# Optimization experiments

Hardware: AMD Instinct MI355X
Metric: run time of the kernel (lower is better)

## Reference

```python
import jax, jax.numpy as jnp
import numpy as np

N_NODES = 10000
N_EDGES = 16384
D = 128            # node_in_dim == out_dim == edge_attr_dim == hidden_dim


def setup_inputs() -> dict:
    key = jax.random.key(0)
    ks = jax.random.split(key, 9)
    s = 1.0 / np.sqrt(D)
    x = jax.random.normal(ks[0], (N_NODES, D), dtype=jnp.float32)
    edge_index = jax.random.randint(ks[1], (2, N_EDGES), 0, N_NODES, dtype=jnp.int64)
    edge_attr = jax.random.normal(ks[2], (N_EDGES, D), dtype=jnp.float32)
    # edge_net: MLP 128 -> 128 (ReLU) -> 128*128
    w1 = jax.random.normal(ks[3], (D, D), dtype=jnp.float32) * s
    b1 = jnp.zeros((D,), dtype=jnp.float32)
    w2 = jax.random.normal(ks[4], (D, D * D), dtype=jnp.float32) * s
    b2 = jnp.zeros((D * D,), dtype=jnp.float32)
    # NNConv root weight and bias
    root = jax.random.normal(ks[5], (D, D), dtype=jnp.float32) * s
    bias = jnp.zeros((D,), dtype=jnp.float32)
    return {"x": x, "edge_index": edge_index, "edge_attr": edge_attr,
            "w1": w1, "b1": b1, "w2": w2, "b2": b2, "root": root, "bias": bias}


def reference(x, edge_index, edge_attr, w1, b1, w2, b2, root, bias):
    src, dst = edge_index[0], edge_index[1]
    # edge_net -> per-edge weight matrices [E, D, D]
    h = jax.nn.relu(edge_attr @ w1 + b1)
    w_edge = (h @ w2 + b2).reshape(-1, D, D)
    # gather source features, per-edge matvec: [E, D]
    x_j = x[src]
    msg = jnp.einsum('ei,eio->eo', x_j, w_edge)
    # scatter-mean into destination nodes
    seg_sum = jax.ops.segment_sum(msg, dst, num_segments=N_NODES)
    cnt = jax.ops.segment_sum(jnp.ones((msg.shape[0],), msg.dtype), dst,
                              num_segments=N_NODES)
    aggr = seg_sum / jnp.maximum(cnt, 1.0)[:, None]
    # NNConv root transform + bias
    conv_out = aggr + x @ root + bias
    # residual + exact GELU (torch nn.GELU default)
    return x + jax.nn.gelu(conv_out, approximate=False)
```

## Files before the change

kernel.cpp:

```cpp
#include <hip/hip_runtime.h>
#include <math.h>

#define D 128
#define NNODES 10000
#define NEDGES 16384
#define PADR 136
#define MAXDEG 16

typedef short short8 __attribute__((ext_vector_type(8)));
typedef float floatx4 __attribute__((ext_vector_type(4)));

__device__ __forceinline__ float bf2f(unsigned short u) {
  union { unsigned u; float f; } v; v.u = ((unsigned)u) << 16; return v.f;
}
__device__ __forceinline__ unsigned short f2bf(float f) {
  union { float f; unsigned u; } v; v.f = f;
  return (unsigned short)((v.u + 0x7FFFu + ((v.u >> 16) & 1u)) >> 16);
}
__device__ __forceinline__ float bflo(unsigned u) {
  union { unsigned u; float f; } v; v.u = u << 16; return v.f;
}
__device__ __forceinline__ float bfhi(unsigned u) {
  union { unsigned u; float f; } v; v.u = u & 0xFFFF0000u; return v.f;
}
__device__ __forceinline__ short8 pack8(float4 a, float4 b) {
  short8 r;
  r[0] = (short)f2bf(a.x); r[1] = (short)f2bf(a.y);
  r[2] = (short)f2bf(a.z); r[3] = (short)f2bf(a.w);
  r[4] = (short)f2bf(b.x); r[5] = (short)f2bf(b.y);
  r[6] = (short)f2bf(b.z); r[7] = (short)f2bf(b.w);
  return r;
}

__global__ __launch_bounds__(256) void k2_prep(
    const float* __restrict__ w2, const float* __restrict__ b2,
    const float* __restrict__ w1, const float* __restrict__ root,
    unsigned short* __restrict__ w2t, unsigned short* __restrict__ w1t,
    unsigned short* __restrict__ rootT) {
  __shared__ float L[32][129];
  const int t = threadIdx.x;
  const int bid = blockIdx.x;
  const float* __restrict__ src;
  unsigned short* dst;
  int o0;
  if (bid < 516) {
    const int k = bid >> 2;
    o0 = (bid & 3) * 32;
    src = (k < D) ? (w2 + (long)k * (D * D)) : b2;
    dst = w2t + (long)k * (D * PADR);
  } else if (bid < 520) {
    o0 = (bid - 516) * 32; src = w1; dst = w1t;
  } else {
    o0 = (bid - 520) * 32; src = root; dst = rootT;
  }
#pragma unroll
  for (int r = 0; r < 16; ++r) {
    int idx = r * 256 + t;
    int i = idx >> 5, oc = idx & 31;
    L[oc][i] = src[i * D + o0 + oc];
  }
  __syncthreads();
#pragma unroll
  for (int r = 0; r < 8; ++r) {
    int p = r * 256 + t;
    int oc = p >> 6, i2 = (p & 63) * 2;
    unsigned v = (unsigned)f2bf(L[oc][i2]) | ((unsigned)f2bf(L[oc][i2 + 1]) << 16);
    *(unsigned*)(dst + ((o0 + oc) * PADR + i2)) = v;
  }
}

__global__ __launch_bounds__(256) void k1_edge(
    const float* __restrict__ x, const int* __restrict__ eidx,
    const float* __restrict__ ea, const unsigned short* __restrict__ w1t,
    const float* __restrict__ b1, unsigned short* __restrict__ hT,
    unsigned short* __restrict__ xjb, int* __restrict__ cnt,
    int* __restrict__ elist) {
  const int t = threadIdx.x;
  const int e0 = blockIdx.x * 64;
  if (t < 64) {
    const int e = e0 + t;
    const int d = eidx[NEDGES + e];
    const int pos = atomicAdd(&cnt[d], 1);
    if (pos < MAXDEG) elist[d * MAXDEG + pos] = e;
  }
#pragma unroll 4
  for (int r = 0; r < 16; ++r) {
    int idx = r * 256 + t, e = idx >> 6, i2 = (idx & 63) * 2;
    const int s = eidx[e0 + e];
    const float2 v = *(const float2*)(x + (long)s * D + i2);
    unsigned p = (unsigned)f2bf(v.x) | ((unsigned)f2bf(v.y) << 16);
    *(unsigned*)(xjb + ((e0 + e) * PADR + i2)) = p;
  }
  const int lane = t & 63, w = t >> 6, lo = lane & 15, hi = lane >> 4;
  short8 af[4];
#pragma unroll
  for (int ks = 0; ks < 4; ++ks) {
    const float* p0 = ea + (long)(e0 + w * 16 + lo) * D + ks * 32 + hi * 8;
    af[ks] = pack8(*(const float4*)p0, *(const float4*)(p0 + 4));
  }
  floatx4 acc[8];
#pragma unroll
  for (int nt = 0; nt < 8; ++nt) acc[nt] = (floatx4){0.f, 0.f, 0.f, 0.f};
#pragma unroll
  for (int ks = 0; ks < 4; ++ks) {
    const int ib = ks * 32 + hi * 8;
#pragma unroll
    for (int nt = 0; nt < 8; ++nt) {
      const short8 bf_ = *(const short8*)&w1t[(nt * 16 + lo) * PADR + ib];
      acc[nt] = __builtin_amdgcn_mfma_f32_16x16x32_bf16(af[ks], bf_, acc[nt], 0, 0, 0);
    }
  }
#pragma unroll
  for (int nt = 0; nt < 8; ++nt) {
    const int ko = nt * 16 + lo;
    const float b1v = b1[ko];
    float v0 = fmaxf(acc[nt][0] + b1v, 0.f);
    float v1 = fmaxf(acc[nt][1] + b1v, 0.f);
    float v2 = fmaxf(acc[nt][2] + b1v, 0.f);
    float v3 = fmaxf(acc[nt][3] + b1v, 0.f);
    uint2 pk;
    pk.x = (unsigned)f2bf(v0) | ((unsigned)f2bf(v1) << 16);
    pk.y = (unsigned)f2bf(v2) | ((unsigned)f2bf(v3) << 16);
    *(uint2*)(hT + (ko * NEDGES + e0 + w * 16 + hi * 4)) = pk;
  }
  if (t < 64) hT[128 * NEDGES + e0 + t] = 0x3F80;
}

__global__ __launch_bounds__(256, 3) void k3_msg(
    const unsigned short* __restrict__ w2t,
    const unsigned short* __restrict__ xjb,
    const unsigned short* __restrict__ hT,
    unsigned short* __restrict__ msgout) {
  __shared__ float hLT[65 * 128];
  const int t = threadIdx.x;
  const int b = blockIdx.x;
  const int kh = b & 1;
  const int oq = (b >> 1) & 3;
  const int eg = b >> 3;
  const int e0 = eg * 128;
  const int o0 = oq * 32;
  const int kbase = kh * 64;
  const int kcnt = kh ? 65 : 64;
  const int lane = t & 63, wv = t >> 6;
  const int lo = lane & 15, hi = lane >> 4;
  const int we = (wv >> 1) * 64;
  const int wo = (wv & 1) * 16;

  for (int idx = t; idx < kcnt * 64; idx += 256) {
    const int kk = idx >> 6, e2 = (idx & 63) * 2;
    const unsigned u = *(const unsigned*)&hT[(long)(kbase + kk) * NEDGES + e0 + e2];
    const int ebase = kk * 128;
#pragma unroll
    for (int q = 0; q < 2; ++q) {
      const int e = e2 + q;
      hLT[ebase + ((e >> 6) << 6) + ((e & 15) << 2) + ((e >> 4) & 3)] =
          q ? bfhi(u) : bflo(u);
    }
  }

  short8 xf[4][4];
#pragma unroll
  for (int ne = 0; ne < 4; ++ne)
#pragma unroll
    for (int ks = 0; ks < 4; ++ks)
      xf[ne][ks] = *(const short8*)&xjb[(long)(e0 + we + ne * 16 + lo) * PADR + ks * 32 + hi * 8];
  __syncthreads();

  const long kstride = (long)D * PADR;
  const unsigned short* ap = w2t + (long)kbase * kstride + (long)(o0 + wo + lo) * PADR + hi * 8;
  const float* hp = hLT + we + lo * 4;
  short8 a0[4], a1[4];
#pragma unroll
  for (int ks = 0; ks < 4; ++ks) a0[ks] = *(const short8*)(ap + ks * 32);
#pragma unroll
  for (int ks = 0; ks < 4; ++ks) a1[ks] = *(const short8*)(ap + kstride + ks * 32);
  floatx4 msg[4];
#pragma unroll
  for (int ne = 0; ne < 4; ++ne) msg[ne] = (floatx4){0.f, 0.f, 0.f, 0.f};

  auto body = [&](short8* fr, int k) {
    const floatx4 h4 = *(const floatx4*)(hp + k * 128);
    floatx4 P[4];
#pragma unroll
    for (int ne = 0; ne < 4; ++ne) P[ne] = (floatx4){0.f, 0.f, 0.f, 0.f};
#pragma unroll
    for (int ks = 0; ks < 4; ++ks)
#pragma unroll
      for (int ne = 0; ne < 4; ++ne)
        P[ne] = __builtin_amdgcn_mfma_f32_16x16x32_bf16(fr[ks], xf[ne][ks], P[ne], 0, 0, 0);
#pragma unroll
    for (int ne = 0; ne < 4; ++ne)
#pragma unroll
      for (int r = 0; r < 4; ++r) msg[ne][r] += h4[ne] * P[ne][r];
  };

  const int kpairs = kcnt >> 1;
  for (int j = 0; j < kpairs; ++j) {
    const int k = j * 2;
    body(a0, k);
    {
      const int kp = (k + 2 < kcnt) ? k + 2 : 0;
#pragma unroll
      for (int ks = 0; ks < 4; ++ks)
        a0[ks] = *(const short8*)(ap + (long)kp * kstride + ks * 32);
    }
    body(a1, k + 1);
    {
      const int kp = (k + 3 < kcnt) ? k + 3 : 0;
#pragma unroll
      for (int ks = 0; ks < 4; ++ks)
        a1[ks] = *(const short8*)(ap + (long)kp * kstride + ks * 32);
    }
  }
  if (kcnt & 1) body(a0, kcnt - 1);

#pragma unroll
  for (int ne = 0; ne < 4; ++ne) {
    const long e = e0 + we + ne * 16 + lo;
    uint2 pk;
    pk.x = (unsigned)f2bf(msg[ne][0]) | ((unsigned)f2bf(msg[ne][1]) << 16);
    pk.y = (unsigned)f2bf(msg[ne][2]) | ((unsigned)f2bf(msg[ne][3]) << 16);
    *(uint2*)(msgout + ((long)kh * NEDGES + e) * D + o0 + wo + hi * 4) = pk;
  }
}

__global__ __launch_bounds__(256) void k4_out(
    const float* __restrict__ x, const unsigned short* __restrict__ rootT,
    const float* __restrict__ bias, const unsigned short* __restrict__ msg,
    const int* __restrict__ cnt, const int* __restrict__ elist,
    float* __restrict__ out) {
  __shared__ float segL[64 * 132];
  const int t = threadIdx.x;
  const int n0 = blockIdx.x * 64;
  {
    const int ln = t >> 2;
    const int n = n0 + ln;
    const int oq = (t & 3) * 32;
    float a[32];
#pragma unroll
    for (int i = 0; i < 32; ++i) a[i] = 0.f;
    if (n < NNODES) {
      const int deg = min(cnt[n], MAXDEG);
      for (int j = 0; j < deg; ++j) {
        const int e = elist[n * MAXDEG + j];
        const unsigned short* r0 = msg + (long)e * D + oq;
        const unsigned short* r1 = r0 + (long)NEDGES * D;
#pragma unroll
        for (int q = 0; q < 4; ++q) {
          const uint4 u0 = *(const uint4*)(r0 + q * 8);
          const uint4 u1 = *(const uint4*)(r1 + q * 8);
          a[q * 8 + 0] += bflo(u0.x) + bflo(u1.x);
          a[q * 8 + 1] += bfhi(u0.x) + bfhi(u1.x);
          a[q * 8 + 2] += bflo(u0.y) + bflo(u1.y);
          a[q * 8 + 3] += bfhi(u0.y) + bfhi(u1.y);
          a[q * 8 + 4] += bflo(u0.z) + bflo(u1.z);
          a[q * 8 + 5] += bfhi(u0.z) + bfhi(u1.z);
          a[q * 8 + 6] += bflo(u0.w) + bflo(u1.w);
          a[q * 8 + 7] += bfhi(u0.w) + bfhi(u1.w);
        }
      }
    }
#pragma unroll
    for (int q = 0; q < 8; ++q)
      *(float4*)&segL[ln * 132 + oq + q * 4] =
          (float4){a[q * 4], a[q * 4 + 1], a[q * 4 + 2], a[q * 4 + 3]};
  }
  __syncthreads();
  const int lane = t & 63, w = t >> 6, lo = lane & 15, hi = lane >> 4;
  const int nrow = n0 + w * 16 + lo;
  short8 af[4];
#pragma unroll
  for (int ks = 0; ks < 4; ++ks) {
    if (nrow < NNODES) {
      const float* p0 = x + (long)nrow * D + ks * 32 + hi * 8;
      af[ks] = pack8(*(const float4*)p0, *(const float4*)(p0 + 4));
    } else {
      af[ks] = (short8){0, 0, 0, 0, 0, 0, 0, 0};
    }
  }
  floatx4 acc[8];
#pragma unroll
  for (int nt = 0; nt < 8; ++nt) acc[nt] = (floatx4){0.f, 0.f, 0.f, 0.f};
#pragma unroll
  for (int ks = 0; ks < 4; ++ks) {
    const int ib = ks * 32 + hi * 8;
#pragma unroll
    for (int nt = 0; nt < 8; ++nt) {
      const short8 bf_ = *(const short8*)&rootT[(nt * 16 + lo) * PADR + ib];
      acc[nt] = __builtin_amdgcn_mfma_f32_16x16x32_bf16(af[ks], bf_, acc[nt], 0, 0, 0);
    }
  }
  float dinv[4];
#pragma unroll
  for (int r = 0; r < 4; ++r) {
    const int n = n0 + w * 16 + hi * 4 + r;
    dinv[r] = (n < NNODES) ? 1.0f / fmaxf((float)cnt[n], 1.0f) : 0.f;
  }
#pragma unroll
  for (int nt = 0; nt < 8; ++nt) {
    const int co = nt * 16 + lo;
    const float bv = bias[co];
#pragma unroll
    for (int r = 0; r < 4; ++r) {
      const int n = n0 + w * 16 + hi * 4 + r;
      if (n < NNODES) {
        const float aggr = segL[(w * 16 + hi * 4 + r) * 132 + co] * dinv[r];
        const float v = acc[nt][r] + aggr + bv;
        const float ge = 0.5f * v * (1.0f + erff(v * 0.70710678f));
        out[(long)n * D + co] = x[(long)n * D + co] + ge;
      }
    }
  }
}

extern "C" void kernel_launch(void* const* d_in, const int* in_sizes, int n_in,
                              void* d_out, int out_size, void* d_ws, size_t ws_size,
                              hipStream_t stream) {
  (void)in_sizes; (void)n_in; (void)out_size; (void)ws_size;
  const float* x    = (const float*)d_in[0];
  const int*   eidx = (const int*)d_in[1];
  const float* ea   = (const float*)d_in[2];
  const float* w1   = (const float*)d_in[3];
  const float* b1   = (const float*)d_in[4];
  const float* w2   = (const float*)d_in[5];
  const float* b2   = (const float*)d_in[6];
  const float* root = (const float*)d_in[7];
  const float* bias = (const float*)d_in[8];
  float* out = (float*)d_out;
  char* ws = (char*)d_ws;
  unsigned short* hT    = (unsigned short*)(ws + 0);
  unsigned short* xjb   = (unsigned short*)(ws + 4227072);
  unsigned short* w2t   = (unsigned short*)(ws + 8683520);
  unsigned short* msg   = (unsigned short*)(ws + 13174784);
  int*            cnt   = (int*)(ws + 21563392);
  int*            elist = (int*)(ws + 21603392);
  unsigned short* w1t   = (unsigned short*)(ws + 22243392);
  unsigned short* rootT = (unsigned short*)(ws + 22278208);
  hipMemsetAsync(cnt, 0, 40000, stream);
  hipLaunchKernelGGL(k2_prep, dim3(524), dim3(256), 0, stream,
                     w2, b2, w1, root, w2t, w1t, rootT);
  hipLaunchKernelGGL(k1_edge, dim3(NEDGES / 64), dim3(256), 0, stream,
                     x, eidx, ea, w1t, b1, hT, xjb, cnt, elist);
  hipLaunchKernelGGL(k3_msg, dim3(1024), dim3(256), 0, stream,
                     w2t, xjb, hT, msg);
  hipLaunchKernelGGL(k4_out, dim3((NNODES + 63) / 64), dim3(256), 0, stream,
                     x, rootT, bias, msg, cnt, elist, out);
}
```

Before: 185.5 us.

## Split k3 over input halves instead of hidden halves, widen k4 grid by output quarters

The message kernel now splits work across blocks by input-dimension half, not hidden-unit half. Each block runs all 129 hidden units with half the K-depth MFMAs. The hidden activations are stored in LDS as bf16 rather than fp32 to fit, and occupancy rises to 4 blocks per SM, with s_setprio set around the MFMA burst. The output kernel is split into four output-column quarters per 64-node tile, giving four times as many blocks with fewer registers each. The cost is that the x rows, root weights and edge lists are read redundantly by each quarter.

```diff
diff --git a/kernel.cpp b/kernel.cpp
--- a/kernel.cpp
+++ b/kernel.cpp
@@ -9,6 +9,7 @@
 
 typedef short short8 __attribute__((ext_vector_type(8)));
 typedef float floatx4 __attribute__((ext_vector_type(4)));
+typedef unsigned short ushortx4 __attribute__((ext_vector_type(4)));
 
 __device__ __forceinline__ float bf2f(unsigned short u) {
   union { unsigned u; float f; } v; v.u = ((unsigned)u) << 16; return v.f;
@@ -126,93 +127,93 @@
   if (t < 64) hT[128 * NEDGES + e0 + t] = 0x3F80;
 }
 
-__global__ __launch_bounds__(256, 3) void k3_msg(
+__global__ __launch_bounds__(256, 4) void k3_msg(
     const unsigned short* __restrict__ w2t,
     const unsigned short* __restrict__ xjb,
     const unsigned short* __restrict__ hT,
     unsigned short* __restrict__ msgout) {
-  __shared__ float hLT[65 * 128];
+  __shared__ unsigned short hLT[129 * 128];
   const int t = threadIdx.x;
   const int b = blockIdx.x;
-  const int kh = b & 1;
+  const int ih = b & 1;
   const int oq = (b >> 1) & 3;
   const int eg = b >> 3;
   const int e0 = eg * 128;
   const int o0 = oq * 32;
-  const int kbase = kh * 64;
-  const int kcnt = kh ? 65 : 64;
   const int lane = t & 63, wv = t >> 6;
   const int lo = lane & 15, hi = lane >> 4;
   const int we = (wv >> 1) * 64;
   const int wo = (wv & 1) * 16;
 
-  for (int idx = t; idx < kcnt * 64; idx += 256) {
+  for (int idx = t; idx < 129 * 64; idx += 256) {
     const int kk = idx >> 6, e2 = (idx & 63) * 2;
-    const unsigned u = *(const unsigned*)&hT[(long)(kbase + kk) * NEDGES + e0 + e2];
-    const int ebase = kk * 128;
-#pragma unroll
-    for (int q = 0; q < 2; ++q) {
-      const int e = e2 + q;
-      hLT[ebase + ((e >> 6) << 6) + ((e & 15) << 2) + ((e >> 4) & 3)] =
-          q ? bfhi(u) : bflo(u);
-    }
-  }
-
-  short8 xf[4][4];
+    const unsigned u = *(const unsigned*)&hT[(long)kk * NEDGES + e0 + e2];
+    const int kb = kk * 128 + ((e2 >> 6) << 6);
+    hLT[kb + ((e2 & 15) << 2) + ((e2 >> 4) & 3)] = (unsigned short)(u & 0xFFFFu);
+    const int e3 = e2 + 1;
+    hLT[kb + ((e3 & 15) << 2) + ((e3 >> 4) & 3)] = (unsigned short)(u >> 16);
+  }
+
+  short8 xf[4][2];
 #pragma unroll
   for (int ne = 0; ne < 4; ++ne)
 #pragma unroll
-    for (int ks = 0; ks < 4; ++ks)
-      xf[ne][ks] = *(const short8*)&xjb[(long)(e0 + we + ne * 16 + lo) * PADR + ks * 32 + hi * 8];
+    for (int ks = 0; ks < 2; ++ks)
+      xf[ne][ks] = *(const short8*)&xjb[(long)(e0 + we + ne * 16 + lo) * PADR +
+                                        ih * 64 + ks * 32 + hi * 8];
   __syncthreads();
 
   const long kstride = (long)D * PADR;
-  const unsigned short* ap = w2t + (long)kbase * kstride + (long)(o0 + wo + lo) * PADR + hi * 8;
-  const float* hp = hLT + we + lo * 4;
-  short8 a0[4], a1[4];
-#pragma unroll
-  for (int ks = 0; ks < 4; ++ks) a0[ks] = *(const short8*)(ap + ks * 32);
-#pragma unroll
-  for (int ks = 0; ks < 4; ++ks) a1[ks] = *(const short8*)(ap + kstride + ks * 32);
+  const unsigned short* ap = w2t + (long)(o0 + wo + lo) * PADR + ih * 64 + hi * 8;
+  const unsigned short* hp = hLT + we + lo * 4;
+  short8 a0[2], a1[2];
+#pragma unroll
+  for (int ks = 0; ks < 2; ++ks) a0[ks] = *(const short8*)(ap + ks * 32);
+#pragma unroll
+  for (int ks = 0; ks < 2; ++ks) a1[ks] = *(const short8*)(ap + kstride + ks * 32);
   floatx4 msg[4];
 #pragma unroll
   for (int ne = 0; ne < 4; ++ne) msg[ne] = (floatx4){0.f, 0.f, 0.f, 0.f};
 
   auto body = [&](short8* fr, int k) {
-    const floatx4 h4 = *(const floatx4*)(hp + k * 128);
+    const ushortx4 hu = *(const ushortx4*)(hp + k * 128);
     floatx4 P[4];
 #pragma unroll
     for (int ne = 0; ne < 4; ++ne) P[ne] = (floatx4){0.f, 0.f, 0.f, 0.f};
-#pragma unroll
-    for (int ks = 0; ks < 4; ++ks)
+    __builtin_amdgcn_s_setprio(1);
+#pragma unroll
+    for (int ks = 0; ks < 2; ++ks)
 #pragma unroll
       for (int ne = 0; ne < 4; ++ne)
         P[ne] = __builtin_amdgcn_mfma_f32_16x16x32_bf16(fr[ks], xf[ne][ks], P[ne], 0, 0, 0);
+    __builtin_amdgcn_s_setprio(0);
+    float hv[4];
+#pragma unroll
+    for (int ne = 0; ne < 4; ++ne) hv[ne] = bf2f(hu[ne]);
 #pragma unroll
     for (int ne = 0; ne < 4; ++ne)
 #pragma unroll
-      for (int r = 0; r < 4; ++r) msg[ne][r] += h4[ne] * P[ne][r];
+      for (int r = 0; r < 4; ++r) msg[ne][r] += hv[ne] * P[ne][r];
   };
 
-  const int kpairs = kcnt >> 1;
-  for (int j = 0; j < kpairs; ++j) {
+  for (int j = 0; j < 64; ++j) {
     const int k = j * 2;
     body(a0, k);
     {
-      const int kp = (k + 2 < kcnt) ? k + 2 : 0;
-#pragma unroll
-      for (int ks = 0; ks < 4; ++ks)
+      const int kp = k + 2;
+#pragma unroll
+      for (int ks = 0; ks < 2; ++ks)
         a0[ks] = *(const short8*)(ap + (long)kp * kstride + ks * 32);
     }
     body(a1, k + 1);
     {
-      const int kp = (k + 3 < kcnt) ? k + 3 : 0;
-#pragma unroll
-      for (int ks = 0; ks < 4; ++ks)
+      const int kp = (k + 3 < 129) ? k + 3 : 0;
+#pragma unroll
+      for (int ks = 0; ks < 2; ++ks)
         a1[ks] = *(const short8*)(ap + (long)kp * kstride + ks * 32);
     }
   }
-  if (kcnt & 1) body(a0, kcnt - 1);
+  body(a0, 128);
 
 #pragma unroll
   for (int ne = 0; ne < 4; ++ne) {
@@ -220,7 +221,7 @@
     uint2 pk;
     pk.x = (unsigned)f2bf(msg[ne][0]) | ((unsigned)f2bf(msg[ne][1]) << 16);
     pk.y = (unsigned)f2bf(msg[ne][2]) | ((unsigned)f2bf(msg[ne][3]) << 16);
-    *(uint2*)(msgout + ((long)kh * NEDGES + e) * D + o0 + wo + hi * 4) = pk;
+    *(uint2*)(msgout + ((long)ih * NEDGES + e) * D + o0 + wo + hi * 4) = pk;
   }
 }
 
@@ -229,41 +230,38 @@
     const float* __restrict__ bias, const unsigned short* __restrict__ msg,
     const int* __restrict__ cnt, const int* __restrict__ elist,
     float* __restrict__ out) {
-  __shared__ float segL[64 * 132];
+  __shared__ float segL[64 * 36];
   const int t = threadIdx.x;
-  const int n0 = blockIdx.x * 64;
+  const int bid = blockIdx.x;
+  const int n0 = (bid >> 2) * 64;
+  const int oq = (bid & 3) * 32;
   {
     const int ln = t >> 2;
     const int n = n0 + ln;
-    const int oq = (t & 3) * 32;
-    float a[32];
-#pragma unroll
-    for (int i = 0; i < 32; ++i) a[i] = 0.f;
+    const int os = (t & 3) * 8;
+    float a[8];
+#pragma unroll
+    for (int i = 0; i < 8; ++i) a[i] = 0.f;
     if (n < NNODES) {
       const int deg = min(cnt[n], MAXDEG);
       for (int j = 0; j < deg; ++j) {
         const int e = elist[n * MAXDEG + j];
-        const unsigned short* r0 = msg + (long)e * D + oq;
+        const unsigned short* r0 = msg + (long)e * D + oq + os;
         const unsigned short* r1 = r0 + (long)NEDGES * D;
-#pragma unroll
-        for (int q = 0; q < 4; ++q) {
-          const uint4 u0 = *(const uint4*)(r0 + q * 8);
-          const uint4 u1 = *(const uint4*)(r1 + q * 8);
-          a[q * 8 + 0] += bflo(u0.x) + bflo(u1.x);
-          a[q * 8 + 1] += bfhi(u0.x) + bfhi(u1.x);
-          a[q * 8 + 2] += bflo(u0.y) + bflo(u1.y);
-          a[q * 8 + 3] += bfhi(u0.y) + bfhi(u1.y);
-          a[q * 8 + 4] += bflo(u0.z) + bflo(u1.z);
-          a[q * 8 + 5] += bfhi(u0.z) + bfhi(u1.z);
-          a[q * 8 + 6] += bflo(u0.w) + bflo(u1.w);
-          a[q * 8 + 7] += bfhi(u0.w) + bfhi(u1.w);
-        }
+        const uint4 u0 = *(const uint4*)r0;
+        const uint4 u1 = *(const uint4*)r1;
+        a[0] += bflo(u0.x) + bflo(u1.x);
+        a[1] += bfhi(u0.x) + bfhi(u1.x);
+        a[2] += bflo(u0.y) + bflo(u1.y);
+        a[3] += bfhi(u0.y) + bfhi(u1.y);
+        a[4] += bflo(u0.z) + bflo(u1.z);
+        a[5] += bfhi(u0.z) + bfhi(u1.z);
+        a[6] += bflo(u0.w) + bflo(u1.w);
+        a[7] += bfhi(u0.w) + bfhi(u1.w);
       }
     }
-#pragma unroll
-    for (int q = 0; q < 8; ++q)
-      *(float4*)&segL[ln * 132 + oq + q * 4] =
-          (float4){a[q * 4], a[q * 4 + 1], a[q * 4 + 2], a[q * 4 + 3]};
+    *(float4*)&segL[ln * 36 + os] = (float4){a[0], a[1], a[2], a[3]};
+    *(float4*)&segL[ln * 36 + os + 4] = (float4){a[4], a[5], a[6], a[7]};
   }
   __syncthreads();
   const int lane = t & 63, w = t >> 6, lo = lane & 15, hi = lane >> 4;
@@ -278,15 +276,15 @@
       af[ks] = (short8){0, 0, 0, 0, 0, 0, 0, 0};
     }
   }
-  floatx4 acc[8];
-#pragma unroll
-  for (int nt = 0; nt < 8; ++nt) acc[nt] = (floatx4){0.f, 0.f, 0.f, 0.f};
+  floatx4 acc[2];
+#pragma unroll
+  for (int nt = 0; nt < 2; ++nt) acc[nt] = (floatx4){0.f, 0.f, 0.f, 0.f};
 #pragma unroll
   for (int ks = 0; ks < 4; ++ks) {
     const int ib = ks * 32 + hi * 8;
 #pragma unroll
-    for (int nt = 0; nt < 8; ++nt) {
-      const short8 bf_ = *(const short8*)&rootT[(nt * 16 + lo) * PADR + ib];
+    for (int nt = 0; nt < 2; ++nt) {
+      const short8 bf_ = *(const short8*)&rootT[(oq + nt * 16 + lo) * PADR + ib];
       acc[nt] = __builtin_amdgcn_mfma_f32_16x16x32_bf16(af[ks], bf_, acc[nt], 0, 0, 0);
     }
   }
@@ -297,14 +295,15 @@
     dinv[r] = (n < NNODES) ? 1.0f / fmaxf((float)cnt[n], 1.0f) : 0.f;
   }
 #pragma unroll
-  for (int nt = 0; nt < 8; ++nt) {
-    const int co = nt * 16 + lo;
+  for (int nt = 0; nt < 2; ++nt) {
+    const int col = nt * 16 + lo;
+    const int co = oq + col;
     const float bv = bias[co];
 #pragma unroll
     for (int r = 0; r < 4; ++r) {
       const int n = n0 + w * 16 + hi * 4 + r;
       if (n < NNODES) {
-        const float aggr = segL[(w * 16 + hi * 4 + r) * 132 + co] * dinv[r];
+        const float aggr = segL[(w * 16 + hi * 4 + r) * 36 + col] * dinv[r];
         const float v = acc[nt][r] + aggr + bv;
         const float ge = 0.5f * v * (1.0f + erff(v * 0.70710678f));
         out[(long)n * D + co] = x[(long)n * D + co] + ge;
@@ -343,6 +342,6 @@
                      x, eidx, ea, w1t, b1, hT, xjb, cnt, elist);
   hipLaunchKernelGGL(k3_msg, dim3(1024), dim3(256), 0, stream,
                      w2t, xjb, hT, msg);
-  hipLaunchKernelGGL(k4_out, dim3((NNODES + 63) / 64), dim3(256), 0, stream,
+  hipLaunchKernelGGL(k4_out, dim3(628), dim3(256), 0, stream,
                      x, rootT, bias, msg, cnt, elist, out);
 }
```

New measurement: 194.2 us. 1.05x slower.

## Scatter messages with float atomics in msg kernel instead of edge-list gather

Applied to the files above, without the earlier changes.

The message kernel now atomically adds each per-edge message into a float aggregation buffer indexed by destination node. This removes the bf16 message buffer, the per-node edge lists and the gather loop in the output kernel. The hidden-activation tile in shared memory is stored as bf16 instead of fp32, and the memset is folded into the prep kernel, which also zeroes the aggregation buffer. In exchange it issues many global float atomics (two k-halves and repeated destinations contend), the summation order is no longer deterministic, and the old cap of 16 edges per node no longer applies.

```diff
diff --git a/kernel.cpp b/kernel.cpp
--- a/kernel.cpp
+++ b/kernel.cpp
@@ -5,10 +5,10 @@
 #define NNODES 10000
 #define NEDGES 16384
 #define PADR 136
-#define MAXDEG 16
 
 typedef short short8 __attribute__((ext_vector_type(8)));
 typedef float floatx4 __attribute__((ext_vector_type(4)));
+typedef unsigned short ushortx4 __attribute__((ext_vector_type(4)));
 
 __device__ __forceinline__ float bf2f(unsigned short u) {
   union { unsigned u; float f; } v; v.u = ((unsigned)u) << 16; return v.f;
@@ -36,10 +36,18 @@
     const float* __restrict__ w2, const float* __restrict__ b2,
     const float* __restrict__ w1, const float* __restrict__ root,
     unsigned short* __restrict__ w2t, unsigned short* __restrict__ w1t,
-    unsigned short* __restrict__ rootT) {
+    unsigned short* __restrict__ rootT, int* __restrict__ cnt,
+    float* __restrict__ aggr) {
   __shared__ float L[32][129];
   const int t = threadIdx.x;
   const int bid = blockIdx.x;
+  {
+    const int gid = bid * 256 + t;
+    if (gid < NNODES) cnt[gid] = 0;
+    float4* a4 = (float4*)aggr;
+    for (int i = gid; i < NNODES * (D / 4); i += 524 * 256)
+      a4[i] = (float4){0.f, 0.f, 0.f, 0.f};
+  }
   const float* __restrict__ src;
   unsigned short* dst;
   int o0;
@@ -73,15 +81,13 @@
     const float* __restrict__ x, const int* __restrict__ eidx,
     const float* __restrict__ ea, const unsigned short* __restrict__ w1t,
     const float* __restrict__ b1, unsigned short* __restrict__ hT,
-    unsigned short* __restrict__ xjb, int* __restrict__ cnt,
-    int* __restrict__ elist) {
+    unsigned short* __restrict__ xjb, int* __restrict__ cnt) {
   const int t = threadIdx.x;
   const int e0 = blockIdx.x * 64;
   if (t < 64) {
     const int e = e0 + t;
     const int d = eidx[NEDGES + e];
-    const int pos = atomicAdd(&cnt[d], 1);
-    if (pos < MAXDEG) elist[d * MAXDEG + pos] = e;
+    atomicAdd(&cnt[d], 1);
   }
 #pragma unroll 4
   for (int r = 0; r < 16; ++r) {
@@ -130,8 +136,9 @@
     const unsigned short* __restrict__ w2t,
     const unsigned short* __restrict__ xjb,
     const unsigned short* __restrict__ hT,
-    unsigned short* __restrict__ msgout) {
-  __shared__ float hLT[65 * 128];
+    const int* __restrict__ eidx,
+    float* __restrict__ aggr) {
+  __shared__ unsigned short hLT[65 * 128];
   const int t = threadIdx.x;
   const int b = blockIdx.x;
   const int kh = b & 1;
@@ -146,16 +153,18 @@
   const int we = (wv >> 1) * 64;
   const int wo = (wv & 1) * 16;
 
+  int dstn[4];
+#pragma unroll
+  for (int ne = 0; ne < 4; ++ne)
+    dstn[ne] = eidx[NEDGES + e0 + we + ne * 16 + lo];
+
   for (int idx = t; idx < kcnt * 64; idx += 256) {
     const int kk = idx >> 6, e2 = (idx & 63) * 2;
     const unsigned u = *(const unsigned*)&hT[(long)(kbase + kk) * NEDGES + e0 + e2];
-    const int ebase = kk * 128;
-#pragma unroll
-    for (int q = 0; q < 2; ++q) {
-      const int e = e2 + q;
-      hLT[ebase + ((e >> 6) << 6) + ((e & 15) << 2) + ((e >> 4) & 3)] =
-          q ? bfhi(u) : bflo(u);
-    }
+    const int kb = kk * 128 + ((e2 >> 6) << 6);
+    hLT[kb + ((e2 & 15) << 2) + ((e2 >> 4) & 3)] = (unsigned short)(u & 0xFFFFu);
+    const int e3 = e2 + 1;
+    hLT[kb + ((e3 & 15) << 2) + ((e3 >> 4) & 3)] = (unsigned short)(u >> 16);
   }
 
   short8 xf[4][4];
@@ -168,7 +177,7 @@
 
   const long kstride = (long)D * PADR;
   const unsigned short* ap = w2t + (long)kbase * kstride + (long)(o0 + wo + lo) * PADR + hi * 8;
-  const float* hp = hLT + we + lo * 4;
+  const unsigned short* hp = hLT + we + lo * 4;
   short8 a0[4], a1[4];
 #pragma unroll
   for (int ks = 0; ks < 4; ++ks) a0[ks] = *(const short8*)(ap + ks * 32);
@@ -179,7 +188,7 @@
   for (int ne = 0; ne < 4; ++ne) msg[ne] = (floatx4){0.f, 0.f, 0.f, 0.f};
 
   auto body = [&](short8* fr, int k) {
-    const floatx4 h4 = *(const floatx4*)(hp + k * 128);
+    const ushortx4 hu = *(const ushortx4*)(hp + k * 128);
     floatx4 P[4];
 #pragma unroll
     for (int ne = 0; ne < 4; ++ne) P[ne] = (floatx4){0.f, 0.f, 0.f, 0.f};
@@ -189,9 +198,11 @@
       for (int ne = 0; ne < 4; ++ne)
         P[ne] = __builtin_amdgcn_mfma_f32_16x16x32_bf16(fr[ks], xf[ne][ks], P[ne], 0, 0, 0);
 #pragma unroll
-    for (int ne = 0; ne < 4; ++ne)
-#pragma unroll
-      for (int r = 0; r < 4; ++r) msg[ne][r] += h4[ne] * P[ne][r];
+    for (int ne = 0; ne < 4; ++ne) {
+      const float hv = bf2f(hu[ne]);
+#pragma unroll
+      for (int r = 0; r < 4; ++r) msg[ne][r] += hv * P[ne][r];
+    }
   };
 
   const int kpairs = kcnt >> 1;
@@ -215,57 +226,18 @@
   if (kcnt & 1) body(a0, kcnt - 1);
 
 #pragma unroll
-  for (int ne = 0; ne < 4; ++ne) {
-    const long e = e0 + we + ne * 16 + lo;
-    uint2 pk;
-    pk.x = (unsigned)f2bf(msg[ne][0]) | ((unsigned)f2bf(msg[ne][1]) << 16);
-    pk.y = (unsigned)f2bf(msg[ne][2]) | ((unsigned)f2bf(msg[ne][3]) << 16);
-    *(uint2*)(msgout + ((long)kh * NEDGES + e) * D + o0 + wo + hi * 4) = pk;
-  }
+  for (int ne = 0; ne < 4; ++ne)
+#pragma unroll
+    for (int r = 0; r < 4; ++r)
+      atomicAdd(&aggr[(long)dstn[ne] * D + o0 + wo + hi * 4 + r], msg[ne][r]);
 }
 
 __global__ __launch_bounds__(256) void k4_out(
     const float* __restrict__ x, const unsigned short* __restrict__ rootT,
-    const float* __restrict__ bias, const unsigned short* __restrict__ msg,
-    const int* __restrict__ cnt, const int* __restrict__ elist,
-    float* __restrict__ out) {
-  __shared__ float segL[64 * 132];
+    const float* __restrict__ bias, const float* __restrict__ aggr,
+    const int* __restrict__ cnt, float* __restrict__ out) {
   const int t = threadIdx.x;
   const int n0 = blockIdx.x * 64;
-  {
-    const int ln = t >> 2;
-    const int n = n0 + ln;
-    const int oq = (t & 3) * 32;
-    float a[32];
-#pragma unroll
-    for (int i = 0; i < 32; ++i) a[i] = 0.f;
-    if (n < NNODES) {
-      const int deg = min(cnt[n], MAXDEG);
-      for (int j = 0; j < deg; ++j) {
-        const int e = elist[n * MAXDEG + j];
-        const unsigned short* r0 = msg + (long)e * D + oq;
-        const unsigned short* r1 = r0 + (long)NEDGES * D;
-#pragma unroll
-        for (int q = 0; q < 4; ++q) {
-          const uint4 u0 = *(const uint4*)(r0 + q * 8);
-          const uint4 u1 = *(const uint4*)(r1 + q * 8);
-          a[q * 8 + 0] += bflo(u0.x) + bflo(u1.x);
-          a[q * 8 + 1] += bfhi(u0.x) + bfhi(u1.x);
-          a[q * 8 + 2] += bflo(u0.y) + bflo(u1.y);
-          a[q * 8 + 3] += bfhi(u0.y) + bfhi(u1.y);
-          a[q * 8 + 4] += bflo(u0.z) + bflo(u1.z);
-          a[q * 8 + 5] += bfhi(u0.z) + bfhi(u1.z);
-          a[q * 8 + 6] += bflo(u0.w) + bflo(u1.w);
-          a[q * 8 + 7] += bfhi(u0.w) + bfhi(u1.w);
-        }
-      }
-    }
-#pragma unroll
-    for (int q = 0; q < 8; ++q)
-      *(float4*)&segL[ln * 132 + oq + q * 4] =
-          (float4){a[q * 4], a[q * 4 + 1], a[q * 4 + 2], a[q * 4 + 3]};
-  }
-  __syncthreads();
   const int lane = t & 63, w = t >> 6, lo = lane & 15, hi = lane >> 4;
   const int nrow = n0 + w * 16 + lo;
   short8 af[4];
@@ -304,8 +276,8 @@
     for (int r = 0; r < 4; ++r) {
       const int n = n0 + w * 16 + hi * 4 + r;
       if (n < NNODES) {
-        const float aggr = segL[(w * 16 + hi * 4 + r) * 132 + co] * dinv[r];
-        const float v = acc[nt][r] + aggr + bv;
+        const float aggv = aggr[(long)n * D + co] * dinv[r];
+        const float v = acc[nt][r] + aggv + bv;
         const float ge = 0.5f * v * (1.0f + erff(v * 0.70710678f));
         out[(long)n * D + co] = x[(long)n * D + co] + ge;
       }
@@ -331,18 +303,16 @@
   unsigned short* hT    = (unsigned short*)(ws + 0);
   unsigned short* xjb   = (unsigned short*)(ws + 4227072);
   unsigned short* w2t   = (unsigned short*)(ws + 8683520);
-  unsigned short* msg   = (unsigned short*)(ws + 13174784);
-  int*            cnt   = (int*)(ws + 21563392);
-  int*            elist = (int*)(ws + 21603392);
-  unsigned short* w1t   = (unsigned short*)(ws + 22243392);
-  unsigned short* rootT = (unsigned short*)(ws + 22278208);
-  hipMemsetAsync(cnt, 0, 40000, stream);
+  float*          aggr  = (float*)(ws + 13174784);
+  int*            cnt   = (int*)(ws + 18294784);
+  unsigned short* w1t   = (unsigned short*)(ws + 18334784);
+  unsigned short* rootT = (unsigned short*)(ws + 18369600);
   hipLaunchKernelGGL(k2_prep, dim3(524), dim3(256), 0, stream,
-                     w2, b2, w1, root, w2t, w1t, rootT);
+                     w2, b2, w1, root, w2t, w1t, rootT, cnt, aggr);
   hipLaunchKernelGGL(k1_edge, dim3(NEDGES / 64), dim3(256), 0, stream,
-                     x, eidx, ea, w1t, b1, hT, xjb, cnt, elist);
+                     x, eidx, ea, w1t, b1, hT, xjb, cnt);
   hipLaunchKernelGGL(k3_msg, dim3(1024), dim3(256), 0, stream,
-                     w2t, xjb, hT, msg);
+                     w2t, xjb, hT, eidx, aggr);
   hipLaunchKernelGGL(k4_out, dim3((NNODES + 63) / 64), dim3(256), 0, stream,
-                     x, rootT, bias, msg, cnt, elist, out);
-}
+                     x, rootT, bias, aggr, cnt, out);
+}
```

After: 221.9 us. +19.6%, slower.

## Merge prep and edge kernels, move degree bucketing into message kernel

Applied to the files above, without the earlier changes.

Fuses the weight-transpose prep kernel and the edge MLP kernel into one launch with block-range dispatch. The memset of the count array is folded into the first blocks, and each edge block converts w1 to bf16 in its own shared memory instead of reading a global prepared copy. Destination degree counting and edge-list building move into the message kernel. This removes two launches and a memset. The cost is redundant w1 conversion in every edge block and larger shared memory use. The count zeroing now relies on it finishing in the previous kernel before the message kernel's atomics.

```diff
diff --git a/kernel.cpp b/kernel.cpp
--- a/kernel.cpp
+++ b/kernel.cpp
@@ -9,6 +9,7 @@
 
 typedef short short8 __attribute__((ext_vector_type(8)));
 typedef float floatx4 __attribute__((ext_vector_type(4)));
+typedef unsigned short ushortx4 __attribute__((ext_vector_type(4)));
 
 __device__ __forceinline__ float bf2f(unsigned short u) {
   union { unsigned u; float f; } v; v.u = ((unsigned)u) << 16; return v.f;
@@ -32,57 +33,51 @@
   return r;
 }
 
-__global__ __launch_bounds__(256) void k2_prep(
+__global__ __launch_bounds__(256) void k12(
+    const float* __restrict__ x, const int* __restrict__ eidx,
+    const float* __restrict__ ea,
+    const float* __restrict__ w1, const float* __restrict__ b1,
     const float* __restrict__ w2, const float* __restrict__ b2,
-    const float* __restrict__ w1, const float* __restrict__ root,
-    unsigned short* __restrict__ w2t, unsigned short* __restrict__ w1t,
-    unsigned short* __restrict__ rootT) {
+    const float* __restrict__ root,
+    unsigned short* __restrict__ w2t, unsigned short* __restrict__ rootT,
+    unsigned short* __restrict__ hT, unsigned short* __restrict__ xjb,
+    int* __restrict__ cnt) {
   __shared__ float L[32][129];
+  __shared__ unsigned short w1tL[128 * PADR];
   const int t = threadIdx.x;
   const int bid = blockIdx.x;
-  const float* __restrict__ src;
-  unsigned short* dst;
-  int o0;
-  if (bid < 516) {
-    const int k = bid >> 2;
-    o0 = (bid & 3) * 32;
-    src = (k < D) ? (w2 + (long)k * (D * D)) : b2;
-    dst = w2t + (long)k * (D * PADR);
-  } else if (bid < 520) {
-    o0 = (bid - 516) * 32; src = w1; dst = w1t;
-  } else {
-    o0 = (bid - 520) * 32; src = root; dst = rootT;
-  }
-#pragma unroll
-  for (int r = 0; r < 16; ++r) {
-    int idx = r * 256 + t;
-    int i = idx >> 5, oc = idx & 31;
-    L[oc][i] = src[i * D + o0 + oc];
-  }
-  __syncthreads();
-#pragma unroll
-  for (int r = 0; r < 8; ++r) {
-    int p = r * 256 + t;
-    int oc = p >> 6, i2 = (p & 63) * 2;
-    unsigned v = (unsigned)f2bf(L[oc][i2]) | ((unsigned)f2bf(L[oc][i2 + 1]) << 16);
-    *(unsigned*)(dst + ((o0 + oc) * PADR + i2)) = v;
-  }
-}
-
-__global__ __launch_bounds__(256) void k1_edge(
-    const float* __restrict__ x, const int* __restrict__ eidx,
-    const float* __restrict__ ea, const unsigned short* __restrict__ w1t,
-    const float* __restrict__ b1, unsigned short* __restrict__ hT,
-    unsigned short* __restrict__ xjb, int* __restrict__ cnt,
-    int* __restrict__ elist) {
-  const int t = threadIdx.x;
-  const int e0 = blockIdx.x * 64;
-  if (t < 64) {
-    const int e = e0 + t;
-    const int d = eidx[NEDGES + e];
-    const int pos = atomicAdd(&cnt[d], 1);
-    if (pos < MAXDEG) elist[d * MAXDEG + pos] = e;
-  }
+
+  if (bid < 520) {
+    if (bid < 40) { const int gid = bid * 256 + t; if (gid < NNODES) cnt[gid] = 0; }
+    const float* __restrict__ src;
+    unsigned short* dst;
+    int o0;
+    if (bid < 516) {
+      const int k = bid >> 2;
+      o0 = (bid & 3) * 32;
+      src = (k < D) ? (w2 + (long)k * (D * D)) : b2;
+      dst = w2t + (long)k * (D * PADR);
+    } else {
+      o0 = (bid - 516) * 32; src = root; dst = rootT;
+    }
+#pragma unroll
+    for (int r = 0; r < 16; ++r) {
+      int idx = r * 256 + t;
+      int i = idx >> 5, oc = idx & 31;
+      L[oc][i] = src[i * D + o0 + oc];
+    }
+    __syncthreads();
+#pragma unroll
+    for (int r = 0; r < 8; ++r) {
+      int p = r * 256 + t;
+      int oc = p >> 6, i2 = (p & 63) * 2;
+      unsigned v = (unsigned)f2bf(L[oc][i2]) | ((unsigned)f2bf(L[oc][i2 + 1]) << 16);
+      *(unsigned*)(dst + ((o0 + oc) * PADR + i2)) = v;
+    }
+    return;
+  }
+
+  const int e0 = (bid - 520) * 64;
 #pragma unroll 4
   for (int r = 0; r < 16; ++r) {
     int idx = r * 256 + t, e = idx >> 6, i2 = (idx & 63) * 2;
@@ -91,6 +86,24 @@
     unsigned p = (unsigned)f2bf(v.x) | ((unsigned)f2bf(v.y) << 16);
     *(unsigned*)(xjb + ((e0 + e) * PADR + i2)) = p;
   }
+  for (int c = 0; c < 4; ++c) {
+    const int o0c = c * 32;
+#pragma unroll
+    for (int r = 0; r < 16; ++r) {
+      int idx = r * 256 + t;
+      int i = idx >> 5, oc = idx & 31;
+      L[oc][i] = w1[i * D + o0c + oc];
+    }
+    __syncthreads();
+#pragma unroll
+    for (int r = 0; r < 8; ++r) {
+      int p = r * 256 + t;
+      int oc = p >> 6, i2 = (p & 63) * 2;
+      unsigned v = (unsigned)f2bf(L[oc][i2]) | ((unsigned)f2bf(L[oc][i2 + 1]) << 16);
+      *(unsigned*)(w1tL + ((o0c + oc) * PADR + i2)) = v;
+    }
+    __syncthreads();
+  }
   const int lane = t & 63, w = t >> 6, lo = lane & 15, hi = lane >> 4;
   short8 af[4];
 #pragma unroll
@@ -106,7 +119,7 @@
     const int ib = ks * 32 + hi * 8;
 #pragma unroll
     for (int nt = 0; nt < 8; ++nt) {
-      const short8 bf_ = *(const short8*)&w1t[(nt * 16 + lo) * PADR + ib];
+      const short8 bf_ = *(const short8*)&w1tL[(nt * 16 + lo) * PADR + ib];
       acc[nt] = __builtin_amdgcn_mfma_f32_16x16x32_bf16(af[ks], bf_, acc[nt], 0, 0, 0);
     }
   }
@@ -130,6 +143,8 @@
     const unsigned short* __restrict__ w2t,
     const unsigned short* __restrict__ xjb,
     const unsigned short* __restrict__ hT,
+    const int* __restrict__ eidx, int* __restrict__ cnt,
+    int* __restrict__ elist,
     unsigned short* __restrict__ msgout) {
   __shared__ float hLT[65 * 128];
   const int t = threadIdx.x;
@@ -145,6 +160,13 @@
   const int lo = lane & 15, hi = lane >> 4;
   const int we = (wv >> 1) * 64;
   const int wo = (wv & 1) * 16;
+
+  if ((b & 7) == 0 && t < 128) {
+    const int e = e0 + t;
+    const int d = eidx[NEDGES + e];
+    const int pos = atomicAdd(&cnt[d], 1);
+    if (pos < MAXDEG) elist[d * MAXDEG + pos] = e;
+  }
 
   for (int idx = t; idx < kcnt * 64; idx += 256) {
     const int kk = idx >> 6, e2 = (idx & 63) * 2;
@@ -334,15 +356,11 @@
   unsigned short* msg   = (unsigned short*)(ws + 13174784);
   int*            cnt   = (int*)(ws + 21563392);
   int*            elist = (int*)(ws + 21603392);
-  unsigned short* w1t   = (unsigned short*)(ws + 22243392);
-  unsigned short* rootT = (unsigned short*)(ws + 22278208);
-  hipMemsetAsync(cnt, 0, 40000, stream);
-  hipLaunchKernelGGL(k2_prep, dim3(524), dim3(256), 0, stream,
-                     w2, b2, w1, root, w2t, w1t, rootT);
-  hipLaunchKernelGGL(k1_edge, dim3(NEDGES / 64), dim3(256), 0, stream,
-                     x, eidx, ea, w1t, b1, hT, xjb, cnt, elist);
+  unsigned short* rootT = (unsigned short*)(ws + 22243392);
+  hipLaunchKernelGGL(k12, dim3(776), dim3(256), 0, stream,
+                     x, eidx, ea, w1, b1, w2, b2, root, w2t, rootT, hT, xjb, cnt);
   hipLaunchKernelGGL(k3_msg, dim3(1024), dim3(256), 0, stream,
-                     w2t, xjb, hT, msg);
+                     w2t, xjb, hT, eidx, cnt, elist, msg);
   hipLaunchKernelGGL(k4_out, dim3((NNODES + 63) / 64), dim3(256), 0, stream,
                      x, rootT, bias, msg, cnt, elist, out);
 }
```

Measured after the change: 182.3 us. About the same (-1.8%).
